# Optimization experiments

Hardware: AMD Instinct MI355X
Metric: run time of the kernel (lower is better)

Reference implementation:

```python
import jax, jax.numpy as jnp
import numpy as np

NUM_LAYERS = 2
D_MODEL = 64
D_INNER = 128   # expand * d_model
D_STATE = 128   # min(2*input_size, 256)
DT_RANK = 4     # ceil(d_model / 16)
D_CONV = 4
HIDDEN = 64


def _causal_dwconv(x, w, b):
    # x: [B, L, C], w: [C, K], b: [C]  -- causal depthwise conv (left pad K-1)
    K = w.shape[1]
    L = x.shape[1]
    xp = jnp.pad(x, ((0, 0), (K - 1, 0), (0, 0)))
    y = sum(xp[:, k:k + L, :] * w[:, k][None, None, :] for k in range(K))
    return y + b


def _selective_scan(u, delta, A, B, C, Dp):
    # u, delta: [b,L,d]; A: [d,n]; B, C: [b,L,n]; Dp: [d]
    dA = jnp.exp(jnp.einsum('bld,dn->lbdn', delta, A))          # [L,b,d,n]
    dBu = jnp.einsum('bld,bln,bld->lbdn', delta, B, u)           # [L,b,d,n]
    Ct = jnp.swapaxes(C, 0, 1)                                   # [L,b,n]

    def step(h, inp):
        dA_t, dBu_t, C_t = inp
        h = dA_t * h + dBu_t                                     # [b,d,n]
        y = jnp.einsum('bdn,bn->bd', h, C_t)
        return h, y

    h0 = jnp.zeros(dA.shape[1:], dA.dtype)
    _, ys = jax.lax.scan(step, h0, (dA, dBu, Ct))                # ys: [L,b,d]
    return jnp.swapaxes(ys, 0, 1) + u * Dp


def _mamba_layer(x, in_w, conv_w, conv_b, xproj_w, dt_w, dt_b, A_log, Dp, out_w):
    xz = x @ in_w.T                                              # [B,L,2*d_inner]
    xi, z = jnp.split(xz, 2, axis=-1)
    xi = jax.nn.silu(_causal_dwconv(xi, conv_w, conv_b))
    xdbl = xi @ xproj_w.T                                        # [B,L,dt_rank+2*d_state]
    delta = jax.nn.softplus(xdbl[..., :DT_RANK] @ dt_w.T + dt_b)
    Bm = xdbl[..., DT_RANK:DT_RANK + D_STATE]
    Cm = xdbl[..., DT_RANK + D_STATE:]
    A = -jnp.exp(A_log)
    y = _selective_scan(xi, delta, A, Bm, Cm, Dp)
    y = y * jax.nn.silu(z)
    return y @ out_w.T


def setup_inputs() -> dict:
    key = jax.random.key(0)
    ks = jax.random.split(key, 10)
    B, L = 4, 1024
    s = 0.05
    x = jax.random.normal(ks[0], (B, L, D_MODEL), dtype=jnp.float32)
    in_proj_w = jax.random.normal(ks[1], (NUM_LAYERS, 2 * D_INNER, D_MODEL)) * s
    conv_w = jax.random.normal(ks[2], (NUM_LAYERS, D_INNER, D_CONV)) * 0.2
    conv_b = jax.random.normal(ks[3], (NUM_LAYERS, D_INNER)) * 0.02
    x_proj_w = jax.random.normal(ks[4], (NUM_LAYERS, DT_RANK + 2 * D_STATE, D_INNER)) * s
    dt_w = jax.random.normal(ks[5], (NUM_LAYERS, D_INNER, DT_RANK)) * 0.1
    dt_b = jnp.full((NUM_LAYERS, D_INNER), -4.6, dtype=jnp.float32)  # softplus -> ~0.01
    # S4D-real init: A_log = log(1..d_state)
    A_log = jnp.log(jnp.broadcast_to(
        jnp.arange(1, D_STATE + 1, dtype=jnp.float32), (NUM_LAYERS, D_INNER, D_STATE)))
    D = jnp.ones((NUM_LAYERS, D_INNER), dtype=jnp.float32)
    out_proj_w = jax.random.normal(ks[6], (NUM_LAYERS, D_MODEL, D_INNER)) * s
    fc_w = jax.random.normal(ks[7], (HIDDEN, D_MODEL)) * s
    fc_b = jax.random.normal(ks[8], (HIDDEN,)) * 0.02
    return {"x": x, "in_proj_w": in_proj_w, "conv_w": conv_w, "conv_b": conv_b,
            "x_proj_w": x_proj_w, "dt_w": dt_w, "dt_b": dt_b, "A_log": A_log,
            "D": D, "out_proj_w": out_proj_w, "fc_w": fc_w, "fc_b": fc_b}


def reference(x, in_proj_w, conv_w, conv_b, x_proj_w, dt_w, dt_b, A_log, D, out_proj_w, fc_w, fc_b):
    h = x
    for l in range(NUM_LAYERS):
        h = _mamba_layer(h, in_proj_w[l], conv_w[l], conv_b[l], x_proj_w[l],
                         dt_w[l], dt_b[l], A_log[l], D[l], out_proj_w[l])
    return h @ fc_w.T + fc_b
```

## Files before the change

### kernel.cpp

```cpp
#include <hip/hip_runtime.h>
#include <hip/hip_bf16.h>

#define BB 4
#define LL 1024
#define DM 64
#define DI 128
#define DS 128
#define DTR 4
#define KC 4
#define RT 8
#define GRP 8
#define CS 128
#define NC 8
#define L2E 1.44269504f

#define XWT_OFF   0
#define INWT_OFF  65536
#define OWT_OFF   98304
#define CWT_OFF   114688
#define CB_OFF    115712
#define DTWT_OFF  115968
#define DTB_OFF   116992
#define XWDT_OFF  117248

__device__ __forceinline__ float bf2f(__hip_bfloat16 v) { return __bfloat162float(v); }
__device__ __forceinline__ float silu_f(float x) { return x / (1.f + __expf(-x)); }

__device__ __forceinline__ float ldf(const void* p, long i, unsigned bf) {
    return bf ? __bfloat162float(((const __hip_bfloat16*)p)[i]) : ((const float*)p)[i];
}

__device__ __forceinline__ void fma4(float4& acc, float s, const float4 w) {
    acc.x = fmaf(s, w.x, acc.x); acc.y = fmaf(s, w.y, acc.y);
    acc.z = fmaf(s, w.z, acc.z); acc.w = fmaf(s, w.w, acc.w);
}

__device__ __forceinline__ void probe_flags(const void* dtb, const void* fcw,
                                            unsigned& bfe, unsigned& bfw) {
    unsigned w = *(const unsigned*)dtb;
    bfe = (w == 0xC093C093u) ? 1u : 0u;
    const unsigned* p = (const unsigned*)fcw;
    int cnt = 0;
    for (int i = 0; i < 32; ++i) {
        unsigned m = p[i] & 0x7FFFu;
        if (m >= 0x3000u && m < 0x4200u) cnt++;
    }
    bfw = (cnt >= 28) ? 1u : 0u;
}

__global__ __launch_bounds__(256) void k_prep(
        const void* __restrict__ inw, const void* __restrict__ xw,
        const void* __restrict__ ow, const void* __restrict__ cw,
        const void* __restrict__ cb, const void* __restrict__ dtw,
        const void* __restrict__ dtb, const void* __restrict__ fcw,
        unsigned* __restrict__ flags, float* __restrict__ WT) {
    unsigned bfe, bfw;
    probe_flags(dtb, fcw, bfe, bfw);
    int bid = blockIdx.x, tid = threadIdx.x;
    if (bid < 28) {
        const void* src; long soff; int srcK; float* dst; int dstN; int n0, k0;
        if (bid < 16) {
            int l = bid >> 3, kt = (bid >> 2) & 1, nt = bid & 3;
            src = xw; srcK = 128; soff = (long)l * 260 * 128 + 4 * 128;
            n0 = nt * 64; k0 = kt * 64; dst = WT + XWT_OFF + l * 32768; dstN = 256;
        } else if (bid < 24) {
            int b2 = bid - 16, l = b2 >> 2, nt = b2 & 3;
            src = inw; srcK = 64; soff = (long)l * 256 * 64;
            n0 = nt * 64; k0 = 0; dst = WT + INWT_OFF + l * 16384; dstN = 256;
        } else {
            int b2 = bid - 24, l = b2 >> 1, kt = b2 & 1;
            src = ow; srcK = 128; soff = (long)l * 64 * 128;
            n0 = 0; k0 = kt * 64; dst = WT + OWT_OFF + l * 8192; dstN = 64;
        }
        __shared__ float tile[64 * 65];
        for (int i = tid; i < 4096; i += 256) {
            int ln = i >> 6, lk = i & 63;
            tile[ln * 65 + lk] = ldf(src, soff + (long)(n0 + ln) * srcK + k0 + lk, bfw);
        }
        __syncthreads();
        for (int i = tid; i < 4096; i += 256) {
            int lk = i >> 6, ln = i & 63;
            dst[(long)(k0 + lk) * dstN + n0 + ln] = tile[ln * 65 + lk];
        }
    } else {
        if (tid == 0) { flags[0] = bfe; flags[1] = bfw; flags[2] = bfe & bfw; }
        for (int j = tid; j < 1024; j += 256) {
            int l = j >> 9, t = (j >> 7) & 3, d = j & 127;
            WT[CWT_OFF + j] = ldf(cw, (long)l * 512 + d * 4 + t, bfw);
        }
        for (int j = tid; j < 256; j += 256) WT[CB_OFF + j] = ldf(cb, j, bfw);
        for (int j = tid; j < 1024; j += 256) {
            int l = j >> 9, r = (j >> 7) & 3, d = j & 127;
            WT[DTWT_OFF + j] = ldf(dtw, (long)l * 512 + d * 4 + r, bfw);
        }
        for (int j = tid; j < 256; j += 256) WT[DTB_OFF + j] = ldf(dtb, j, bfe);
        for (int j = tid; j < 1024; j += 256) {
            int l = j >> 9, rem = j & 511;
            WT[XWDT_OFF + j] = ldf(xw, (long)l * 260 * 128 + rem, bfw);
        }
    }
}

__global__ __launch_bounds__(256) void k_inproj(
        const void* __restrict__ xin, int xin_probe,
        const float* __restrict__ wt, const unsigned* __restrict__ flags,
        float* __restrict__ xzx, float* __restrict__ sz) {
    unsigned bfx = xin_probe ? flags[0] : 0u;
    int row0 = blockIdx.x * RT;
    int tid = threadIdx.x, lane = tid & 63, g = tid >> 6;
    __shared__ float act[RT * DM];
    for (int i = tid; i < RT * DM; i += 256)
        act[i] = ldf(xin, (long)(row0 + (i >> 6)) * DM + (i & 63), bfx);
    __syncthreads();
    const float4* wt4 = (const float4*)wt;
    float4 acc[2];
    acc[0] = make_float4(0.f, 0.f, 0.f, 0.f);
    acc[1] = make_float4(0.f, 0.f, 0.f, 0.f);
#pragma unroll 8
    for (int k4 = 0; k4 < DM / 4; ++k4) {
        float4 w0 = wt4[(k4 * 4 + 0) * 64 + lane];
        float4 w1 = wt4[(k4 * 4 + 1) * 64 + lane];
        float4 w2 = wt4[(k4 * 4 + 2) * 64 + lane];
        float4 w3 = wt4[(k4 * 4 + 3) * 64 + lane];
#pragma unroll
        for (int r = 0; r < 2; ++r) {
            float4 av = *(const float4*)&act[(g * 2 + r) * DM + k4 * 4];
            fma4(acc[r], av.x, w0); fma4(acc[r], av.y, w1);
            fma4(acc[r], av.z, w2); fma4(acc[r], av.w, w3);
        }
    }
    int n0 = lane * 4;
#pragma unroll
    for (int r = 0; r < 2; ++r) {
        int row = row0 + g * 2 + r;
        if (n0 < DI) {
            *(float4*)&xzx[(size_t)row * DI + n0] = acc[r];
        } else {
            float4 v;
            v.x = silu_f(acc[r].x); v.y = silu_f(acc[r].y);
            v.z = silu_f(acc[r].z); v.w = silu_f(acc[r].w);
            *(float4*)&sz[(size_t)row * DI + (n0 - DI)] = v;
        }
    }
}

__global__ __launch_bounds__(256) void k_xproj(
        const float* __restrict__ xzx,
        const float* __restrict__ cwT, const float* __restrict__ cbF,
        const float* __restrict__ xwT, const float* __restrict__ xwdtF,
        const float* __restrict__ dtwT, const float* __restrict__ dtbF,
        float* __restrict__ xiw, float* __restrict__ dlt,
        float* __restrict__ Bm, float* __restrict__ Cm) {
    int row0 = blockIdx.x * RT;
    int b = row0 >> 10, l0 = row0 & (LL - 1);
    int tid = threadIdx.x, lane = tid & 63, g = tid >> 6;
    __shared__ float xc[(RT + KC - 1) * DI];
    __shared__ float act[RT * DI];
    __shared__ float dtp[RT * DTR];
    for (int i = tid; i < (RT + KC - 1) * DI; i += 256) {
        int r = (i >> 7) - (KC - 1);
        int l = l0 + r;
        xc[i] = (l >= 0) ? xzx[((size_t)b * LL + l) * DI + (i & 127)] : 0.f;
    }
    __syncthreads();
    for (int i = tid; i < RT * DI; i += 256) {
        int r = i >> 7, d = i & 127;
        float a = cbF[d];
#pragma unroll
        for (int t = 0; t < KC; ++t) a = fmaf(xc[(r + t) * DI + d], cwT[t * DI + d], a);
        float v = silu_f(a);
        act[i] = v;
        xiw[(size_t)(row0 + r) * DI + d] = v;
    }
    __syncthreads();
    const float4* wt4 = (const float4*)xwT;
    float4 acc[2];
    acc[0] = make_float4(0.f, 0.f, 0.f, 0.f);
    acc[1] = make_float4(0.f, 0.f, 0.f, 0.f);
#pragma unroll 8
    for (int k4 = 0; k4 < DI / 4; ++k4) {
        float4 w0 = wt4[(k4 * 4 + 0) * 64 + lane];
        float4 w1 = wt4[(k4 * 4 + 1) * 64 + lane];
        float4 w2 = wt4[(k4 * 4 + 2) * 64 + lane];
        float4 w3 = wt4[(k4 * 4 + 3) * 64 + lane];
#pragma unroll
        for (int r = 0; r < 2; ++r) {
            float4 av = *(const float4*)&act[(g * 2 + r) * DI + k4 * 4];
            fma4(acc[r], av.x, w0); fma4(acc[r], av.y, w1);
            fma4(acc[r], av.z, w2); fma4(acc[r], av.w, w3);
        }
    }
    int n0 = lane * 4;
#pragma unroll
    for (int r = 0; r < 2; ++r) {
        int row = row0 + g * 2 + r;
        if (n0 < DS) *(float4*)&Bm[(size_t)row * DS + n0] = acc[r];
        else         *(float4*)&Cm[(size_t)row * DS + (n0 - DS)] = acc[r];
    }
    if (tid < RT * DTR) {
        int r = tid >> 2, i = tid & 3;
        float a = 0.f;
#pragma unroll
        for (int k4 = 0; k4 < DI / 4; ++k4) {
            float4 av = *(const float4*)&act[r * DI + k4 * 4];
            float4 wv = *(const float4*)&xwdtF[i * DI + k4 * 4];
            a = fmaf(av.x, wv.x, a); a = fmaf(av.y, wv.y, a);
            a = fmaf(av.z, wv.z, a); a = fmaf(av.w, wv.w, a);
        }
        dtp[tid] = a;
    }
    __syncthreads();
    if (tid < DI) {
        float dw0 = dtwT[0 * DI + tid], dw1 = dtwT[1 * DI + tid];
        float dw2 = dtwT[2 * DI + tid], dw3 = dtwT[3 * DI + tid];
        float bv = dtbF[tid];
#pragma unroll
        for (int r = 0; r < RT; ++r) {
            float a = bv;
            a = fmaf(dtp[r * 4 + 0], dw0, a);
            a = fmaf(dtp[r * 4 + 1], dw1, a);
            a = fmaf(dtp[r * 4 + 2], dw2, a);
            a = fmaf(dtp[r * 4 + 3], dw3, a);
            dlt[(size_t)(row0 + r) * DI + tid] = (a > 20.f) ? a : log1pf(__expf(a));
        }
    }
}

__global__ __launch_bounds__(256) void k_scanA(
        const float* __restrict__ dlt, const float* __restrict__ xiw,
        const float* __restrict__ Bm,
        const void* __restrict__ Alog, long aoff,
        const unsigned* __restrict__ flags,
        float* __restrict__ hend, float* __restrict__ S) {
    __shared__ float dsh[CS * 4];
    __shared__ float dush[CS * 4];
    int gid = blockIdx.x;
    int dg = gid / (BB * NC);
    int bc = gid % (BB * NC);
    int b = bc / NC, c = bc % NC;
    int d0 = dg * 4;
    int tid = threadIdx.x;
    int w = tid >> 6, t = tid & 63;
    int d = d0 + w;
    int c0 = c * CS;
    unsigned bfe = flags[0];
    float A0 = -L2E * __expf(ldf(Alog, aoff + (long)d * DS + 2 * t, bfe));
    float A1 = -L2E * __expf(ldf(Alog, aoff + (long)d * DS + 2 * t + 1, bfe));
    for (int i = tid; i < CS * 4; i += 256) {
        size_t src = ((size_t)b * LL + c0 + (i >> 2)) * DI + d0 + (i & 3);
        float dl = dlt[src];
        dsh[i] = dl;
        dush[i] = dl * xiw[src];
    }
    __syncthreads();
    const float2* Bg = (const float2*)(Bm + ((size_t)b * LL + c0) * DS) + t;
    float h0 = 0.f, h1v = 0.f, sumd = 0.f;
    float2 Ba[GRP], Bb[GRP];
#pragma unroll
    for (int s = 0; s < GRP; ++s) Ba[s] = Bg[(size_t)s * (DS / 2)];
    auto grp = [&](int li, const float2* Bv) {
        float dl[GRP], du[GRP], ea0[GRP], ea1[GRP];
#pragma unroll
        for (int s = 0; s < GRP; ++s) {
            dl[s] = dsh[(li + s) * 4 + w];
            du[s] = dush[(li + s) * 4 + w];
        }
#pragma unroll
        for (int s = 0; s < GRP; ++s) {
            ea0[s] = exp2f(dl[s] * A0);
            ea1[s] = exp2f(dl[s] * A1);
        }
#pragma unroll
        for (int s = 0; s < GRP; ++s) {
            h0  = fmaf(ea0[s], h0,  du[s] * Bv[s].x);
            h1v = fmaf(ea1[s], h1v, du[s] * Bv[s].y);
            sumd += dl[s];
        }
    };
    for (int li = 0; li < CS; li += 2 * GRP) {
#pragma unroll
        for (int s = 0; s < GRP; ++s) Bb[s] = Bg[(size_t)(li + GRP + s) * (DS / 2)];
        grp(li, Ba);
        if (li + 2 * GRP < CS) {
#pragma unroll
            for (int s = 0; s < GRP; ++s) Ba[s] = Bg[(size_t)(li + 2 * GRP + s) * (DS / 2)];
        }
        grp(li + GRP, Bb);
    }
    size_t hbase = (((size_t)b * DI + d) * NC + c) * DS;
    ((float2*)(hend + hbase))[t] = make_float2(h0, h1v);
    if (t == 0) S[((size_t)b * DI + d) * NC + c] = sumd;
}

__global__ __launch_bounds__(256) void k_scanC(
        const float* __restrict__ dlt, const float* __restrict__ xiw,
        const float* __restrict__ Bm, const float* __restrict__ Cm,
        const void* __restrict__ Alog, long aoff,
        const void* __restrict__ Dp, long doff,
        const unsigned* __restrict__ flags,
        const float* __restrict__ hend, const float* __restrict__ S,
        float* __restrict__ y) {
    __shared__ float dsh[CS * 4];
    __shared__ float ush[CS * 4];
    __shared__ float dush[CS * 4];
    __shared__ float ysh[CS * 4];
    __shared__ float Wred[4 * 520];
    int gid = blockIdx.x;
    int dg = gid / (BB * NC);
    int bc = gid % (BB * NC);
    int b = bc / NC, c = bc % NC;
    int d0 = dg * 4;
    int tid = threadIdx.x;
    int w = tid >> 6, t = tid & 63;
    int d = d0 + w;
    int c0 = c * CS;
    unsigned bfe = flags[0];
    float A0 = -L2E * __expf(ldf(Alog, aoff + (long)d * DS + 2 * t, bfe));
    float A1 = -L2E * __expf(ldf(Alog, aoff + (long)d * DS + 2 * t + 1, bfe));
    float Dv = ldf(Dp, doff + d, bfe);
    for (int i = tid; i < CS * 4; i += 256) {
        size_t src = ((size_t)b * LL + c0 + (i >> 2)) * DI + d0 + (i & 3);
        float dl = dlt[src];
        float ul = xiw[src];
        dsh[i] = dl;
        ush[i] = ul;
        dush[i] = dl * ul;
    }
    __syncthreads();
    float h0 = 0.f, h1v = 0.f;
    const float2* hep = (const float2*)(hend + (((size_t)b * DI + d) * NC) * DS);
    const float* Sp = S + ((size_t)b * DI + d) * NC;
    for (int cc = 0; cc < c; ++cc) {
        float2 he = hep[(size_t)cc * (DS / 2) + t];
        float s = Sp[cc];
        h0  = fmaf(exp2f(A0 * s), h0,  he.x);
        h1v = fmaf(exp2f(A1 * s), h1v, he.y);
    }
    const float2* Bg = (const float2*)(Bm + ((size_t)b * LL + c0) * DS) + t;
    const float2* Cg = (const float2*)(Cm + ((size_t)b * LL + c0) * DS) + t;
    float* Wl = Wred + w * 520;
    int rbase = (t >> 3) * 65 + (t & 7) * 8;
    float2 Ba[GRP], Ca[GRP], Bb[GRP], Cb[GRP];
#pragma unroll
    for (int s = 0; s < GRP; ++s) {
        Ba[s] = Bg[(size_t)s * (DS / 2)];
        Ca[s] = Cg[(size_t)s * (DS / 2)];
    }
    auto grp = [&](int li, const float2* Bv, const float2* Cv) {
        float dl[GRP], du[GRP], ea0[GRP], ea1[GRP], cv[GRP];
#pragma unroll
        for (int s = 0; s < GRP; ++s) {
            dl[s] = dsh[(li + s) * 4 + w];
            du[s] = dush[(li + s) * 4 + w];
        }
#pragma unroll
        for (int s = 0; s < GRP; ++s) {
            ea0[s] = exp2f(dl[s] * A0);
            ea1[s] = exp2f(dl[s] * A1);
        }
#pragma unroll
        for (int s = 0; s < GRP; ++s) {
            h0  = fmaf(ea0[s], h0,  du[s] * Bv[s].x);
            h1v = fmaf(ea1[s], h1v, du[s] * Bv[s].y);
            cv[s] = fmaf(h0, Cv[s].x, h1v * Cv[s].y);
        }
#pragma unroll
        for (int s = 0; s < GRP; ++s) Wl[s * 65 + t] = cv[s];
        float pt = 0.f;
#pragma unroll
        for (int j = 0; j < 8; ++j) pt += Wl[rbase + j];
        pt += __shfl_xor(pt, 1, 64);
        pt += __shfl_xor(pt, 2, 64);
        pt += __shfl_xor(pt, 4, 64);
        if ((t & 7) == 0) {
            int l = li + (t >> 3);
            ysh[l * 4 + w] = pt + ush[l * 4 + w] * Dv;
        }
    };
    for (int li = 0; li < CS; li += 2 * GRP) {
#pragma unroll
        for (int s = 0; s < GRP; ++s) {
            Bb[s] = Bg[(size_t)(li + GRP + s) * (DS / 2)];
            Cb[s] = Cg[(size_t)(li + GRP + s) * (DS / 2)];
        }
        grp(li, Ba, Ca);
        if (li + 2 * GRP < CS) {
#pragma unroll
            for (int s = 0; s < GRP; ++s) {
                Ba[s] = Bg[(size_t)(li + 2 * GRP + s) * (DS / 2)];
                Ca[s] = Cg[(size_t)(li + 2 * GRP + s) * (DS / 2)];
            }
        }
        grp(li + GRP, Bb, Cb);
    }
    __syncthreads();
    for (int i = tid; i < CS * 4; i += 256)
        y[((size_t)b * LL + c0 + (i >> 2)) * DI + d0 + (i & 3)] = ysh[i];
}

__global__ __launch_bounds__(256) void k_out(
        const float* __restrict__ y, const float* __restrict__ sz,
        const float* __restrict__ owT, float* __restrict__ hout) {
    int row0 = blockIdx.x * RT;
    int tid = threadIdx.x, n = tid & 63, g = tid >> 6;
    __shared__ float act[RT * DI];
    for (int i = tid; i < RT * DI; i += 256) {
        size_t idx = (size_t)(row0 + (i >> 7)) * DI + (i & 127);
        act[i] = y[idx] * sz[idx];
    }
    __syncthreads();
    float acc[2] = {0.f, 0.f};
#pragma unroll 8
    for (int k4 = 0; k4 < DI / 4; ++k4) {
        float w0 = owT[(k4 * 4 + 0) * DM + n];
        float w1 = owT[(k4 * 4 + 1) * DM + n];
        float w2 = owT[(k4 * 4 + 2) * DM + n];
        float w3 = owT[(k4 * 4 + 3) * DM + n];
#pragma unroll
        for (int r = 0; r < 2; ++r) {
            float4 av = *(const float4*)&act[(g * 2 + r) * DI + k4 * 4];
            acc[r] = fmaf(av.x, w0, acc[r]); acc[r] = fmaf(av.y, w1, acc[r]);
            acc[r] = fmaf(av.z, w2, acc[r]); acc[r] = fmaf(av.w, w3, acc[r]);
        }
    }
#pragma unroll
    for (int r = 0; r < 2; ++r)
        hout[(size_t)(row0 + g * 2 + r) * DM + n] = acc[r];
}

__global__ __launch_bounds__(256) void k_fc(
        const float* __restrict__ h, const void* __restrict__ fw,
        const void* __restrict__ fb, const unsigned* __restrict__ flags,
        void* __restrict__ out) {
    unsigned bfw = flags[1], obf = flags[2];
    int row0 = blockIdx.x * RT;
    int tid = threadIdx.x, n = tid & 63, g = tid >> 6;
    __shared__ float wsh[DM * 65];
    __shared__ float act[RT * DM];
    for (int i = tid; i < DM * DM; i += 256) {
        int nn = i >> 6, k = i & 63;
        wsh[k * 65 + nn] = ldf(fw, i, bfw);
    }
    for (int i = tid; i < RT * DM; i += 256)
        act[i] = h[(size_t)(row0 + (i >> 6)) * DM + (i & 63)];
    __syncthreads();
    float bv = ldf(fb, n, bfw);
    float acc[2] = {bv, bv};
#pragma unroll 8
    for (int k4 = 0; k4 < DM / 4; ++k4) {
        float w0 = wsh[(k4 * 4 + 0) * 65 + n];
        float w1 = wsh[(k4 * 4 + 1) * 65 + n];
        float w2 = wsh[(k4 * 4 + 2) * 65 + n];
        float w3 = wsh[(k4 * 4 + 3) * 65 + n];
#pragma unroll
        for (int r = 0; r < 2; ++r) {
            float4 av = *(const float4*)&act[(g * 2 + r) * DM + k4 * 4];
            acc[r] = fmaf(av.x, w0, acc[r]); acc[r] = fmaf(av.y, w1, acc[r]);
            acc[r] = fmaf(av.z, w2, acc[r]); acc[r] = fmaf(av.w, w3, acc[r]);
        }
    }
#pragma unroll
    for (int r = 0; r < 2; ++r) {
        size_t idx = (size_t)(row0 + g * 2 + r) * DM + n;
        if (obf) ((__hip_bfloat16*)out)[idx] = __float2bfloat16(acc[r]);
        else     ((float*)out)[idx] = acc[r];
    }
}

extern "C" void kernel_launch(void* const* d_in, const int* in_sizes, int n_in,
                              void* d_out, int out_size, void* d_ws, size_t ws_size,
                              hipStream_t stream) {
    const void* x    = d_in[0];
    const void* inw  = d_in[1];
    const void* cw   = d_in[2];
    const void* cb   = d_in[3];
    const void* xw   = d_in[4];
    const void* dtw  = d_in[5];
    const void* dtb  = d_in[6];
    const void* Alog = d_in[7];
    const void* Dp   = d_in[8];
    const void* ow   = d_in[9];
    const void* fcw  = d_in[10];
    const void* fcb  = d_in[11];

    const size_t NBL = (size_t)BB * LL;
    const int GB = (int)(NBL / RT);
    const bool big = ws_size >= (size_t)18 * 1024 * 1024;
    unsigned* flags = (unsigned*)d_ws;
    float* base = (float*)d_ws + 64;
    float *h1, *S, *sz, *xiw, *dlt, *Bmw, *Cmw, *hend, *yw, *xzx;
    if (big) {
        h1   = base;
        sz   = h1 + 262144;
        xiw  = sz + 524288;
        dlt  = xiw + 524288;
        Bmw  = dlt + 524288;
        Cmw  = Bmw + 524288;
        yw   = Cmw + 524288;
        hend = yw + 524288;
        S    = hend + 524288;
        xzx  = yw;
    } else {
        xzx  = base;
        h1   = base + 524288;
        S    = h1;
        sz   = base + 786432;
        xiw  = sz + 524288;
        dlt  = xiw + 524288;
        Bmw  = dlt + 524288;
        Cmw  = Bmw + 524288;
        hend = base;
        yw   = dlt;
    }
    float* WT = (float*)d_out;

    k_prep<<<29, 256, 0, stream>>>(inw, xw, ow, cw, cb, dtw, dtb, fcw, flags, WT);

    for (int l = 0; l < 2; ++l) {
        const void* xin = (l == 0) ? x : (const void*)h1;
        int xmode = (l == 0) ? 1 : 0;
        k_inproj<<<GB, 256, 0, stream>>>(xin, xmode, WT + INWT_OFF + l * 16384, flags, xzx, sz);
        k_xproj<<<GB, 256, 0, stream>>>(xzx,
                                        WT + CWT_OFF + l * 512, WT + CB_OFF + l * 128,
                                        WT + XWT_OFF + l * 32768, WT + XWDT_OFF + l * 512,
                                        WT + DTWT_OFF + l * 512, WT + DTB_OFF + l * 128,
                                        xiw, dlt, Bmw, Cmw);
        long ao = (long)l * DI * DS;
        long dof = (long)l * DI;
        k_scanA<<<32 * BB * NC, 256, 0, stream>>>(dlt, xiw, Bmw, Alog, ao, flags, hend, S);
        k_scanC<<<32 * BB * NC, 256, 0, stream>>>(dlt, xiw, Bmw, Cmw, Alog, ao,
                                                  Dp, dof, flags, hend, S, yw);
        k_out<<<GB, 256, 0, stream>>>(yw, sz, WT + OWT_OFF + l * 8192, h1);
    }
    k_fc<<<GB, 256, 0, stream>>>(h1, fcw, fcb, flags, d_out);
}
```

Measured before the change: 300.1 us.

## Fuse chunked scan passes into one cooperative kernel with grid sync

Replaces the two-pass chunked selective scan (state pass then output pass) with a single cooperative kernel. Each block scans its chunk from zero state once, producing both local outputs and the chunk-end state. After a grid-wide sync it adds the carried-in state's contribution using a prefix sum of delta, so B and the recurrence are not recomputed. The kernel is used only if occupancy allows all 1024 blocks to be resident, otherwise it falls back to the old kernels. The change also drops the small-workspace layout path and removes software prefetch double-buffering of B and C from the fallback kernels.

Result: no change. 296.0 us (-1.4%).

```diff
diff --git a/kernel.cpp b/kernel.cpp
--- a/kernel.cpp
+++ b/kernel.cpp
@@ -1,5 +1,8 @@
 #include <hip/hip_runtime.h>
 #include <hip/hip_bf16.h>
+#include <hip/hip_cooperative_groups.h>
+
+namespace cg = cooperative_groups;
 
 #define BB 4
 #define LL 1024
@@ -226,14 +229,19 @@
     }
 }
 
-__global__ __launch_bounds__(256) void k_scanA(
+__global__ __launch_bounds__(256) void k_scanF(
         const float* __restrict__ dlt, const float* __restrict__ xiw,
-        const float* __restrict__ Bm,
+        const float* __restrict__ Bm, const float* __restrict__ Cm,
         const void* __restrict__ Alog, long aoff,
+        const void* __restrict__ Dp, long doff,
         const unsigned* __restrict__ flags,
-        float* __restrict__ hend, float* __restrict__ S) {
+        float* __restrict__ hend, float* __restrict__ S,
+        float* __restrict__ y) {
     __shared__ float dsh[CS * 4];
     __shared__ float dush[CS * 4];
+    __shared__ float cdsh[CS * 4];
+    __shared__ float ysh[CS * 4];
+    __shared__ float Wred[4 * 520];
     int gid = blockIdx.x;
     int dg = gid / (BB * NC);
     int bc = gid % (BB * NC);
@@ -249,21 +257,157 @@
     for (int i = tid; i < CS * 4; i += 256) {
         size_t src = ((size_t)b * LL + c0 + (i >> 2)) * DI + d0 + (i & 3);
         float dl = dlt[src];
+        float ul = xiw[src];
         dsh[i] = dl;
-        dush[i] = dl * xiw[src];
+        dush[i] = dl * ul;
+        ysh[i] = ul * ldf(Dp, doff + d0 + (i & 3), bfe);
+    }
+    __syncthreads();
+    {
+        float a = dsh[t * 4 + w];
+        float bb2 = dsh[(64 + t) * 4 + w];
+#pragma unroll
+        for (int off = 1; off < 64; off <<= 1) {
+            float n = __shfl(a, t - off, 64);
+            if (t >= off) a += n;
+        }
+        float T1 = __shfl(a, 63, 64);
+#pragma unroll
+        for (int off = 1; off < 64; off <<= 1) {
+            float n = __shfl(bb2, t - off, 64);
+            if (t >= off) bb2 += n;
+        }
+        bb2 += T1;
+        cdsh[t * 4 + w] = a;
+        cdsh[(64 + t) * 4 + w] = bb2;
+    }
+    const float2* Bg = (const float2*)(Bm + ((size_t)b * LL + c0) * DS) + t;
+    const float2* Cg = (const float2*)(Cm + ((size_t)b * LL + c0) * DS) + t;
+    float* Wl = Wred + w * 520;
+    int rbase = (t >> 3) * 65 + (t & 7) * 8;
+    float h0 = 0.f, h1v = 0.f;
+    for (int li = 0; li < CS; li += GRP) {
+        float dl[GRP], du[GRP], ea0[GRP], ea1[GRP], cv[GRP];
+        float2 Bv[GRP], Cv[GRP];
+#pragma unroll
+        for (int s = 0; s < GRP; ++s) {
+            dl[s] = dsh[(li + s) * 4 + w];
+            du[s] = dush[(li + s) * 4 + w];
+            Bv[s] = Bg[(size_t)(li + s) * (DS / 2)];
+            Cv[s] = Cg[(size_t)(li + s) * (DS / 2)];
+        }
+#pragma unroll
+        for (int s = 0; s < GRP; ++s) {
+            ea0[s] = exp2f(dl[s] * A0);
+            ea1[s] = exp2f(dl[s] * A1);
+        }
+#pragma unroll
+        for (int s = 0; s < GRP; ++s) {
+            h0  = fmaf(ea0[s], h0,  du[s] * Bv[s].x);
+            h1v = fmaf(ea1[s], h1v, du[s] * Bv[s].y);
+            cv[s] = fmaf(h0, Cv[s].x, h1v * Cv[s].y);
+        }
+#pragma unroll
+        for (int s = 0; s < GRP; ++s) Wl[s * 65 + t] = cv[s];
+        float pt = 0.f;
+#pragma unroll
+        for (int j = 0; j < 8; ++j) pt += Wl[rbase + j];
+        pt += __shfl_xor(pt, 1, 64);
+        pt += __shfl_xor(pt, 2, 64);
+        pt += __shfl_xor(pt, 4, 64);
+        if ((t & 7) == 0) {
+            int l = li + (t >> 3);
+            ysh[l * 4 + w] += pt;
+        }
+    }
+    if (c < NC - 1) {
+        size_t hbase = (((size_t)b * DI + d) * NC + c) * DS;
+        ((float2*)(hend + hbase))[t] = make_float2(h0, h1v);
+        if (t == 0) S[((size_t)b * DI + d) * NC + c] = cdsh[127 * 4 + w];
+    }
+    __threadfence();
+    cg::this_grid().sync();
+    if (c > 0) {
+        float hi0 = 0.f, hi1 = 0.f;
+        const float2* hep = (const float2*)(hend + (((size_t)b * DI + d) * NC) * DS);
+        const float* Sp = S + ((size_t)b * DI + d) * NC;
+        for (int cc = 0; cc < c; ++cc) {
+            float2 he = hep[(size_t)cc * (DS / 2) + t];
+            float s = Sp[cc];
+            hi0 = fmaf(exp2f(A0 * s), hi0, he.x);
+            hi1 = fmaf(exp2f(A1 * s), hi1, he.y);
+        }
+        for (int li = 0; li < CS; li += GRP) {
+            float cd[GRP], ea0[GRP], ea1[GRP], cv[GRP];
+            float2 Cv[GRP];
+#pragma unroll
+            for (int s = 0; s < GRP; ++s) {
+                cd[s] = cdsh[(li + s) * 4 + w];
+                Cv[s] = Cg[(size_t)(li + s) * (DS / 2)];
+            }
+#pragma unroll
+            for (int s = 0; s < GRP; ++s) {
+                ea0[s] = exp2f(cd[s] * A0);
+                ea1[s] = exp2f(cd[s] * A1);
+            }
+#pragma unroll
+            for (int s = 0; s < GRP; ++s)
+                cv[s] = fmaf(hi0 * ea0[s], Cv[s].x, hi1 * ea1[s] * Cv[s].y);
+#pragma unroll
+            for (int s = 0; s < GRP; ++s) Wl[s * 65 + t] = cv[s];
+            float pt = 0.f;
+#pragma unroll
+            for (int j = 0; j < 8; ++j) pt += Wl[rbase + j];
+            pt += __shfl_xor(pt, 1, 64);
+            pt += __shfl_xor(pt, 2, 64);
+            pt += __shfl_xor(pt, 4, 64);
+            if ((t & 7) == 0) {
+                int l = li + (t >> 3);
+                ysh[l * 4 + w] += pt;
+            }
+        }
+    }
+    __syncthreads();
+    for (int i = tid; i < CS * 4; i += 256)
+        y[((size_t)b * LL + c0 + (i >> 2)) * DI + d0 + (i & 3)] = ysh[i];
+}
+
+__global__ __launch_bounds__(256) void k_scanA(
+        const float* __restrict__ dlt, const float* __restrict__ xiw,
+        const float* __restrict__ Bm,
+        const void* __restrict__ Alog, long aoff,
+        const unsigned* __restrict__ flags,
+        float* __restrict__ hend, float* __restrict__ S) {
+    __shared__ float dsh[CS * 4];
+    __shared__ float ush[CS * 4];
+    int gid = blockIdx.x;
+    int dg = gid / (BB * NC);
+    int bc = gid % (BB * NC);
+    int b = bc / NC, c = bc % NC;
+    int d0 = dg * 4;
+    int tid = threadIdx.x;
+    int w = tid >> 6, t = tid & 63;
+    int d = d0 + w;
+    int c0 = c * CS;
+    unsigned bfe = flags[0];
+    float A0 = -L2E * __expf(ldf(Alog, aoff + (long)d * DS + 2 * t, bfe));
+    float A1 = -L2E * __expf(ldf(Alog, aoff + (long)d * DS + 2 * t + 1, bfe));
+    for (int i = tid; i < CS * 4; i += 256) {
+        size_t src = ((size_t)b * LL + c0 + (i >> 2)) * DI + d0 + (i & 3);
+        dsh[i] = dlt[src];
+        ush[i] = xiw[src];
     }
     __syncthreads();
     const float2* Bg = (const float2*)(Bm + ((size_t)b * LL + c0) * DS) + t;
     float h0 = 0.f, h1v = 0.f, sumd = 0.f;
-    float2 Ba[GRP], Bb[GRP];
-#pragma unroll
-    for (int s = 0; s < GRP; ++s) Ba[s] = Bg[(size_t)s * (DS / 2)];
-    auto grp = [&](int li, const float2* Bv) {
-        float dl[GRP], du[GRP], ea0[GRP], ea1[GRP];
+    for (int li = 0; li < CS; li += GRP) {
+        float dl[GRP], ul[GRP], ea0[GRP], ea1[GRP];
+        float2 Bv[GRP];
 #pragma unroll
         for (int s = 0; s < GRP; ++s) {
             dl[s] = dsh[(li + s) * 4 + w];
-            du[s] = dush[(li + s) * 4 + w];
+            ul[s] = ush[(li + s) * 4 + w];
+            Bv[s] = Bg[(size_t)(li + s) * (DS / 2)];
         }
 #pragma unroll
         for (int s = 0; s < GRP; ++s) {
@@ -272,20 +416,11 @@
         }
 #pragma unroll
         for (int s = 0; s < GRP; ++s) {
-            h0  = fmaf(ea0[s], h0,  du[s] * Bv[s].x);
-            h1v = fmaf(ea1[s], h1v, du[s] * Bv[s].y);
+            float db = dl[s] * ul[s];
+            h0  = fmaf(ea0[s], h0,  db * Bv[s].x);
+            h1v = fmaf(ea1[s], h1v, db * Bv[s].y);
             sumd += dl[s];
         }
-    };
-    for (int li = 0; li < CS; li += 2 * GRP) {
-#pragma unroll
-        for (int s = 0; s < GRP; ++s) Bb[s] = Bg[(size_t)(li + GRP + s) * (DS / 2)];
-        grp(li, Ba);
-        if (li + 2 * GRP < CS) {
-#pragma unroll
-            for (int s = 0; s < GRP; ++s) Ba[s] = Bg[(size_t)(li + 2 * GRP + s) * (DS / 2)];
-        }
-        grp(li + GRP, Bb);
     }
     size_t hbase = (((size_t)b * DI + d) * NC + c) * DS;
     ((float2*)(hend + hbase))[t] = make_float2(h0, h1v);
@@ -302,7 +437,6 @@
         float* __restrict__ y) {
     __shared__ float dsh[CS * 4];
     __shared__ float ush[CS * 4];
-    __shared__ float dush[CS * 4];
     __shared__ float ysh[CS * 4];
     __shared__ float Wred[4 * 520];
     int gid = blockIdx.x;
@@ -320,11 +454,8 @@
     float Dv = ldf(Dp, doff + d, bfe);
     for (int i = tid; i < CS * 4; i += 256) {
         size_t src = ((size_t)b * LL + c0 + (i >> 2)) * DI + d0 + (i & 3);
-        float dl = dlt[src];
-        float ul = xiw[src];
-        dsh[i] = dl;
-        ush[i] = ul;
-        dush[i] = dl * ul;
+        dsh[i] = dlt[src];
+        ush[i] = xiw[src];
     }
     __syncthreads();
     float h0 = 0.f, h1v = 0.f;
@@ -340,18 +471,15 @@
     const float2* Cg = (const float2*)(Cm + ((size_t)b * LL + c0) * DS) + t;
     float* Wl = Wred + w * 520;
     int rbase = (t >> 3) * 65 + (t & 7) * 8;
-    float2 Ba[GRP], Ca[GRP], Bb[GRP], Cb[GRP];
-#pragma unroll
-    for (int s = 0; s < GRP; ++s) {
-        Ba[s] = Bg[(size_t)s * (DS / 2)];
-        Ca[s] = Cg[(size_t)s * (DS / 2)];
-    }
-    auto grp = [&](int li, const float2* Bv, const float2* Cv) {
-        float dl[GRP], du[GRP], ea0[GRP], ea1[GRP], cv[GRP];
+    for (int li = 0; li < CS; li += GRP) {
+        float dl[GRP], ul[GRP], ea0[GRP], ea1[GRP], cv[GRP];
+        float2 Bv[GRP], Cv[GRP];
 #pragma unroll
         for (int s = 0; s < GRP; ++s) {
             dl[s] = dsh[(li + s) * 4 + w];
-            du[s] = dush[(li + s) * 4 + w];
+            ul[s] = ush[(li + s) * 4 + w];
+            Bv[s] = Bg[(size_t)(li + s) * (DS / 2)];
+            Cv[s] = Cg[(size_t)(li + s) * (DS / 2)];
         }
 #pragma unroll
         for (int s = 0; s < GRP; ++s) {
@@ -360,8 +488,9 @@
         }
 #pragma unroll
         for (int s = 0; s < GRP; ++s) {
-            h0  = fmaf(ea0[s], h0,  du[s] * Bv[s].x);
-            h1v = fmaf(ea1[s], h1v, du[s] * Bv[s].y);
+            float db = dl[s] * ul[s];
+            h0  = fmaf(ea0[s], h0,  db * Bv[s].x);
+            h1v = fmaf(ea1[s], h1v, db * Bv[s].y);
             cv[s] = fmaf(h0, Cv[s].x, h1v * Cv[s].y);
         }
 #pragma unroll
@@ -376,22 +505,6 @@
             int l = li + (t >> 3);
             ysh[l * 4 + w] = pt + ush[l * 4 + w] * Dv;
         }
-    };
-    for (int li = 0; li < CS; li += 2 * GRP) {
-#pragma unroll
-        for (int s = 0; s < GRP; ++s) {
-            Bb[s] = Bg[(size_t)(li + GRP + s) * (DS / 2)];
-            Cb[s] = Cg[(size_t)(li + GRP + s) * (DS / 2)];
-        }
-        grp(li, Ba, Ca);
-        if (li + 2 * GRP < CS) {
-#pragma unroll
-            for (int s = 0; s < GRP; ++s) {
-                Ba[s] = Bg[(size_t)(li + 2 * GRP + s) * (DS / 2)];
-                Ca[s] = Cg[(size_t)(li + 2 * GRP + s) * (DS / 2)];
-            }
-        }
-        grp(li + GRP, Bb, Cb);
     }
     __syncthreads();
     for (int i = tid; i < CS * 4; i += 256)
@@ -485,34 +598,23 @@
 
     const size_t NBL = (size_t)BB * LL;
     const int GB = (int)(NBL / RT);
-    const bool big = ws_size >= (size_t)18 * 1024 * 1024;
     unsigned* flags = (unsigned*)d_ws;
     float* base = (float*)d_ws + 64;
-    float *h1, *S, *sz, *xiw, *dlt, *Bmw, *Cmw, *hend, *yw, *xzx;
-    if (big) {
-        h1   = base;
-        sz   = h1 + 262144;
-        xiw  = sz + 524288;
-        dlt  = xiw + 524288;
-        Bmw  = dlt + 524288;
-        Cmw  = Bmw + 524288;
-        yw   = Cmw + 524288;
-        hend = yw + 524288;
-        S    = hend + 524288;
-        xzx  = yw;
-    } else {
-        xzx  = base;
-        h1   = base + 524288;
-        S    = h1;
-        sz   = base + 786432;
-        xiw  = sz + 524288;
-        dlt  = xiw + 524288;
-        Bmw  = dlt + 524288;
-        Cmw  = Bmw + 524288;
-        hend = base;
-        yw   = dlt;
-    }
-    float* WT = (float*)d_out;
+    float* h1   = base;
+    float* sz   = h1 + 262144;
+    float* xiw  = sz + 524288;
+    float* dlt  = xiw + 524288;
+    float* Bmw  = dlt + 524288;
+    float* Cmw  = Bmw + 524288;
+    float* yw   = Cmw + 524288;
+    float* hend = yw + 524288;
+    float* S    = hend + 524288;
+    float* xzx  = yw;
+    float* WT   = (float*)d_out;
+
+    int nb = 0;
+    hipOccupancyMaxActiveBlocksPerMultiprocessor(&nb, k_scanF, 256, 0);
+    const bool coop = (nb >= 4);
 
     k_prep<<<29, 256, 0, stream>>>(inw, xw, ow, cw, cb, dtw, dtb, fcw, flags, WT);
 
@@ -527,9 +629,22 @@
                                         xiw, dlt, Bmw, Cmw);
         long ao = (long)l * DI * DS;
         long dof = (long)l * DI;
-        k_scanA<<<32 * BB * NC, 256, 0, stream>>>(dlt, xiw, Bmw, Alog, ao, flags, hend, S);
-        k_scanC<<<32 * BB * NC, 256, 0, stream>>>(dlt, xiw, Bmw, Cmw, Alog, ao,
-                                                  Dp, dof, flags, hend, S, yw);
+        if (coop) {
+            const float* dlt_c = dlt; const float* xiw_c = xiw;
+            const float* Bm_c = Bmw; const float* Cm_c = Cmw;
+            const unsigned* fl_c = flags;
+            void* params[] = {
+                (void*)&dlt_c, (void*)&xiw_c, (void*)&Bm_c, (void*)&Cm_c,
+                (void*)&Alog, (void*)&ao, (void*)&Dp, (void*)&dof,
+                (void*)&fl_c, (void*)&hend, (void*)&S, (void*)&yw
+            };
+            hipLaunchCooperativeKernel((const void*)k_scanF, dim3(32 * BB * NC),
+                                       dim3(256), params, 0, stream);
+        } else {
+            k_scanA<<<32 * BB * NC, 256, 0, stream>>>(dlt, xiw, Bmw, Alog, ao, flags, hend, S);
+            k_scanC<<<32 * BB * NC, 256, 0, stream>>>(dlt, xiw, Bmw, Cmw, Alog, ao,
+                                                      Dp, dof, flags, hend, S, yw);
+        }
         k_out<<<GB, 256, 0, stream>>>(yw, sz, WT + OWT_OFF + l * 8192, h1);
     }
     k_fc<<<GB, 256, 0, stream>>>(h1, fcw, fcb, flags, d_out);
```
